# Performance work log

Measured on AMD Instinct MI355X. Metric: run time of the kernel, lower is better.

Reference implementation:

```python
import jax, jax.numpy as jnp
import numpy as np

T = 1_000_000  # sequence length
H = 5          # LSTM hidden size
NC = 4         # number of channel streams (all fed through lstm1, as in the original)


def setup_inputs() -> dict:
    key = jax.random.key(0)
    ks = jax.random.split(key, 14)
    s = 1.0 / np.sqrt(H)  # PyTorch default LSTM/Linear init scale
    u = lambda k, shape: jax.random.uniform(k, shape, jnp.float32, -s, s)
    sf1 = 1.0 / np.sqrt(20.0)
    sf2 = 1.0 / np.sqrt(10.0)
    return {
        "inputs": jax.random.normal(ks[0], (T, 1, NC), jnp.float32),
        # lstm1 layer 0: input_size=1
        "w_ih0": u(ks[1], (4 * H, 1)),
        "w_hh0": u(ks[2], (4 * H, H)),
        "b_ih0": u(ks[3], (4 * H,)),
        "b_hh0": u(ks[4], (4 * H,)),
        # lstm1 layer 1: input_size=H
        "w_ih1": u(ks[5], (4 * H, H)),
        "w_hh1": u(ks[6], (4 * H, H)),
        "b_ih1": u(ks[7], (4 * H,)),
        "b_hh1": u(ks[8], (4 * H,)),
        "fc1_w": jax.random.uniform(ks[9], (10, 20), jnp.float32, -sf1, sf1),
        "fc1_b": jax.random.uniform(ks[10], (10,), jnp.float32, -sf1, sf1),
        "fc2_w": jax.random.uniform(ks[11], (1, 10), jnp.float32, -sf2, sf2),
        "fc2_b": jax.random.uniform(ks[12], (1,), jnp.float32, -sf2, sf2),
    }


def _lstm_layer(x_seq, w_ih, w_hh, b_ih, b_hh):
    """Single PyTorch-style LSTM layer. x_seq: (T, B, in) -> h_seq: (T, B, H)."""
    # Input projection for all timesteps at once (outside the scan).
    gx = jnp.einsum('tbi,gi->tbg', x_seq, w_ih) + b_ih + b_hh  # (T, B, 4H)

    def step(carry, gx_t):
        h, c = carry
        g = gx_t + h @ w_hh.T                      # (B, 4H)
        i, f, gg, o = jnp.split(g, 4, axis=-1)     # PyTorch gate order i,f,g,o
        i = jax.nn.sigmoid(i)
        f = jax.nn.sigmoid(f)
        gg = jnp.tanh(gg)
        o = jax.nn.sigmoid(o)
        c = f * c + i * gg
        h = o * jnp.tanh(c)
        return (h, c), h

    B = x_seq.shape[1]
    z = jnp.zeros((B, H), x_seq.dtype)
    _, h_seq = jax.lax.scan(step, (z, z), gx)
    return h_seq


def reference(inputs, w_ih0, w_hh0, b_ih0, b_hh0, w_ih1, w_hh1, b_ih1, b_hh1,
              fc1_w, fc1_b, fc2_w, fc2_b):
    # Original code runs all 4 channel streams through lstm1 (lstm2-4 unused),
    # so we fold the 4 streams into the LSTM batch dim: (T, 4, 1).
    x = inputs[:, 0, :, None]                      # (T, NC, 1)
    h = _lstm_layer(x, w_ih0, w_hh0, b_ih0, b_hh0)  # (T, NC, H)
    h = _lstm_layer(h, w_ih1, w_hh1, b_ih1, b_hh1)  # (T, NC, H)
    # torch.cat((out1..out4), dim=2) on (T,1,H) slices == channel-major reshape
    out_cat = h.reshape(T, 1, NC * H)              # (T, 1, 20)
    out = out_cat @ fc1_w.T + fc1_b                # (T, 1, 10)
    out = out @ fc2_w.T + fc2_b                    # (T, 1, 1)
    return out
```

## Files before the change

kernel.cpp:

```cpp
#include <hip/hip_runtime.h>

#define T_TOTAL 1000000
#define NCHUNK  9216
#define CLEN    109
#define WARM    24


typedef float v2 __attribute__((ext_vector_type(2)));

#define L2E  1.44269504088896340736f
#define K2   2.88539008177792681472f

__device__ __forceinline__ float bperm(int addr4, float v) {
    return __int_as_float(__builtin_amdgcn_ds_bpermute(addr4, __float_as_int(v)));
}
__device__ __forceinline__ v2 pkfma(v2 a, v2 b, v2 c) {
    return __builtin_elementwise_fma(a, b, c);
}

__global__ __launch_bounds__(64, 1) void lstm_chunks(
    const float* __restrict__ inp,
    const float* __restrict__ wih0,
    const float* __restrict__ whh0,
    const float* __restrict__ bih0,
    const float* __restrict__ bhh0,
    const float* __restrict__ wih1,
    const float* __restrict__ whh1,
    const float* __restrict__ bih1,
    const float* __restrict__ bhh1,
    const float* __restrict__ fc1w,
    const float* __restrict__ fc1b,
    const float* __restrict__ fc2w,
    const float* __restrict__ fc2b,
    float* __restrict__ out)
{
    const int lane = threadIdx.x & 63;
    int cw = lane / 20; if (cw > 2) cw = 2;
    int q  = lane - cw * 20; if (q > 19) q = 19;
    const int b = q / 5;
    const int j = q % 5;
    const int chunk = blockIdx.x * 3 + cw;
    const int base  = cw * 20;

    int gh[5];
    #pragma unroll
    for (int k = 0; k < 5; ++k) gh[k] = (base + b * 5 + k) * 4;
    const int rd5  = (lane + 5)  * 4;
    const int rd10 = (lane + 10) * 4;

    v2 W0x01, W0x23, BB001, BB023, BB101, BB123;
    v2 W0h01[5], W0h23[5], W1a01[5], W1a23[5], W1b01[5], W1b23[5];
    {
        const int r0 = j, r1 = 5 + j, r2 = 10 + j, r3 = 15 + j;
        const v2 s01 = v2{-L2E, -L2E};
        const v2 s23 = v2{-K2,  -L2E};
        W0x01 = s01 * v2{wih0[r0], wih0[r1]};
        W0x23 = s23 * v2{wih0[r2], wih0[r3]};
        BB001 = s01 * v2{bih0[r0] + bhh0[r0], bih0[r1] + bhh0[r1]};
        BB023 = s23 * v2{bih0[r2] + bhh0[r2], bih0[r3] + bhh0[r3]};
        BB101 = s01 * v2{bih1[r0] + bhh1[r0], bih1[r1] + bhh1[r1]};
        BB123 = s23 * v2{bih1[r2] + bhh1[r2], bih1[r3] + bhh1[r3]};
        #pragma unroll
        for (int k = 0; k < 5; ++k) {
            W0h01[k] = s01 * v2{whh0[r0 * 5 + k], whh0[r1 * 5 + k]};
            W0h23[k] = s23 * v2{whh0[r2 * 5 + k], whh0[r3 * 5 + k]};
            W1a01[k] = s01 * v2{wih1[r0 * 5 + k], wih1[r1 * 5 + k]};
            W1a23[k] = s23 * v2{wih1[r2 * 5 + k], wih1[r3 * 5 + k]};
            W1b01[k] = s01 * v2{whh1[r0 * 5 + k], whh1[r1 * 5 + k]};
            W1b23[k] = s23 * v2{whh1[r2 * 5 + k], whh1[r3 * 5 + k]};
        }
    }
    float vb[5] = {0, 0, 0, 0, 0};
    float sc = fc2b[0];
    #pragma unroll
    for (int m = 0; m < 10; ++m) {
        const float f2 = fc2w[m];
        sc = __builtin_fmaf(f2, fc1b[m], sc);
        #pragma unroll
        for (int k = 0; k < 5; ++k)
            vb[k] = __builtin_fmaf(f2, fc1w[m * 20 + b * 5 + k], vb[k]);
    }

    const int o_begin = chunk * CLEN;
    const int warm = (chunk == 0) ? 0 : WARM;

    float C0 = 0.0f, C1 = 0.0f;
    float h0r[5] = {0, 0, 0, 0, 0};
    float h1r[5] = {0, 0, 0, 0, 0};

    auto ldx = [&](int t) -> float {
        const int tt = (t > T_TOTAL - 1) ? (T_TOTAL - 1) : t;
        return inp[(size_t)tt * 4 + b];
    };

    auto cellp = [&](v2 A01, v2 A23, float& C) -> float {
        const float ei = __builtin_amdgcn_exp2f(A01.x);
        const float ef = __builtin_amdgcn_exp2f(A01.y);
        const float eg = __builtin_amdgcn_exp2f(A23.x);
        const float eo = __builtin_amdgcn_exp2f(A23.y);
        const float Di = 1.0f + ei, Df = 1.0f + ef, Dg = 1.0f + eg, Do = 1.0f + eo;
        const float p1 = Di * Df, p2 = Dg * Do, p3 = Df * Do;
        const float r  = __builtin_amdgcn_rcpf(p1 * p2);
        const float f  = (Di * p2) * r;
        const float o  = (p1 * Dg) * r;
        const float tg = __builtin_fmaf(K2, eg, -K2);
        C = __builtin_fmaf(f, C, (tg * p3) * r);
        const float eh = __builtin_amdgcn_exp2f(C);
        return (o * (1.0f - eh)) * __builtin_amdgcn_rcpf(1.0f + eh);
    };

    auto matvec0 = [&](float x, const float (&h)[5], v2& A01, v2& A23) {
        const v2 xx = v2{x, x};
        v2 P01 = pkfma(W0x01, xx, BB001);
        v2 P23 = pkfma(W0x23, xx, BB023);
        const v2 k0 = v2{h[0], h[0]}, k1 = v2{h[1], h[1]};
        const v2 k2 = v2{h[2], h[2]}, k3 = v2{h[3], h[3]};
        const v2 k4 = v2{h[4], h[4]};
        P01 = pkfma(W0h01[0], k0, P01);  v2 Q01 = W0h01[2] * k2;
        P23 = pkfma(W0h23[0], k0, P23);  v2 Q23 = W0h23[2] * k2;
        P01 = pkfma(W0h01[1], k1, P01);  Q01 = pkfma(W0h01[3], k3, Q01);
        P23 = pkfma(W0h23[1], k1, P23);  Q23 = pkfma(W0h23[3], k3, Q23);
        Q01 = pkfma(W0h01[4], k4, Q01);
        Q23 = pkfma(W0h23[4], k4, Q23);
        A01 = P01 + Q01; A23 = P23 + Q23;
    };
    auto matvec1 = [&](const float (&h0)[5], const float (&h1)[5], v2& A01, v2& A23) {
        v2 P01 = BB101, P23 = BB123;
        const v2 g0 = v2{h1[0], h1[0]};
        v2 Q01 = W1b01[0] * g0;
        v2 Q23 = W1b23[0] * g0;
        #pragma unroll
        for (int k = 0; k < 5; ++k) {
            const v2 hk = v2{h0[k], h0[k]};
            P01 = pkfma(W1a01[k], hk, P01);
            P23 = pkfma(W1a23[k], hk, P23);
        }
        #pragma unroll
        for (int k = 1; k < 5; ++k) {
            const v2 gk = v2{h1[k], h1[k]};
            Q01 = pkfma(W1b01[k], gk, Q01);
            Q23 = pkfma(W1b23[k], gk, Q23);
        }
        A01 = P01 + Q01; A23 = P23 + Q23;
    };

    int t = o_begin - warm;
    {
        v2 A01, A23;
        matvec0(ldx(t), h0r, A01, A23);
        const float h0 = cellp(A01, A23, C0);
        #pragma unroll
        for (int k = 0; k < 5; ++k) h0r[k] = bperm(gh[k], h0);
    }
    float xc = ldx(t + 1);

    #define BODY(EMIT)                                                         \
    {                                                                          \
        v2 A01, A23;                                                           \
        matvec1(h0r, h1r, A01, A23);                                           \
        const float h1 = cellp(A01, A23, C1);                                  \
        float h1n[5];                                                          \
        _Pragma("unroll")                                                      \
        for (int k = 0; k < 5; ++k) h1n[k] = bperm(gh[k], h1);                 \
        const float xn = ldx(t + 2);                                           \
        matvec0(xc, h0r, A01, A23);                                            \
        const float h0 = cellp(A01, A23, C0);                                  \
        _Pragma("unroll")                                                      \
        for (int k = 0; k < 5; ++k) h0r[k] = bperm(gh[k], h0);                 \
        xc = xn;                                                               \
        if (EMIT) {                                                            \
            float p = vb[0] * h1n[0];                                          \
            p = __builtin_fmaf(vb[1], h1n[1], p);                              \
            p = __builtin_fmaf(vb[2], h1n[2], p);                              \
            p = __builtin_fmaf(vb[3], h1n[3], p);                              \
            p = __builtin_fmaf(vb[4], h1n[4], p);                              \
            const float u = p + bperm(rd5, p);                                 \
            const float S = u + bperm(rd10, u);                                \
            if (q == 0 && t < T_TOTAL) out[t] = S + sc;                        \
        }                                                                      \
        _Pragma("unroll")                                                      \
        for (int k = 0; k < 5; ++k) h1r[k] = h1n[k];                           \
    }

    for (int i = 0; i < warm; ++i, ++t) BODY(false)
    for (int i = 0; i < CLEN; ++i, ++t) BODY(true)

    #undef BODY
}

extern "C" void kernel_launch(void* const* d_in, const int* in_sizes, int n_in,
                              void* d_out, int out_size, void* d_ws, size_t ws_size,
                              hipStream_t stream) {
    (void)in_sizes; (void)n_in; (void)d_ws; (void)ws_size; (void)out_size;
    lstm_chunks<<<NCHUNK / 3, 64, 0, stream>>>(
        (const float*)d_in[0],  (const float*)d_in[1],  (const float*)d_in[2],
        (const float*)d_in[3],  (const float*)d_in[4],  (const float*)d_in[5],
        (const float*)d_in[6],  (const float*)d_in[7],  (const float*)d_in[8],
        (const float*)d_in[9],  (const float*)d_in[10], (const float*)d_in[11],
        (const float*)d_in[12], (float*)d_out);
}
```

Measured before the change: 181.0 us.

## Replace packed FMA matvecs with scalar FMAs and use fewer, longer chunks

The packed two-wide FMA vector math in the gate matvecs is replaced by plain scalar FMA chains, one accumulator per gate. The chunk decomposition also changes from 9216 chunks of 109 steps with 24 warmup steps to 6144 chunks of 164 steps with 16 warmup steps. Fewer chunks and shorter warmup cut redundant recurrent work but lengthen the serial chain each wave runs. The reduced warmup may also lower accuracy at chunk boundaries, and the scalar code issues roughly twice as many FMA instructions.

```diff
diff --git a/kernel.cpp b/kernel.cpp
--- a/kernel.cpp
+++ b/kernel.cpp
@@ -1,12 +1,10 @@
 #include <hip/hip_runtime.h>
 
 #define T_TOTAL 1000000
-#define NCHUNK  9216
-#define CLEN    109
-#define WARM    24
-
-
-typedef float v2 __attribute__((ext_vector_type(2)));
+#define NCHUNK  6144
+#define CLEN    164
+#define WARM    16
+
 
 #define L2E  1.44269504088896340736f
 #define K2   2.88539008177792681472f
@@ -14,8 +12,8 @@
 __device__ __forceinline__ float bperm(int addr4, float v) {
     return __int_as_float(__builtin_amdgcn_ds_bpermute(addr4, __float_as_int(v)));
 }
-__device__ __forceinline__ v2 pkfma(v2 a, v2 b, v2 c) {
-    return __builtin_elementwise_fma(a, b, c);
+__device__ __forceinline__ float fmaf_(float a, float b, float c) {
+    return __builtin_fmaf(a, b, c);
 }
 
 __global__ __launch_bounds__(64, 1) void lstm_chunks(
@@ -48,26 +46,23 @@
     const int rd5  = (lane + 5)  * 4;
     const int rd10 = (lane + 10) * 4;
 
-    v2 W0x01, W0x23, BB001, BB023, BB101, BB123;
-    v2 W0h01[5], W0h23[5], W1a01[5], W1a23[5], W1b01[5], W1b23[5];
+    float Wx[4], BB0[4], BB1[4];
+    float W0[4][5], Wa[4][5], Wb[4][5];
     {
-        const int r0 = j, r1 = 5 + j, r2 = 10 + j, r3 = 15 + j;
-        const v2 s01 = v2{-L2E, -L2E};
-        const v2 s23 = v2{-K2,  -L2E};
-        W0x01 = s01 * v2{wih0[r0], wih0[r1]};
-        W0x23 = s23 * v2{wih0[r2], wih0[r3]};
-        BB001 = s01 * v2{bih0[r0] + bhh0[r0], bih0[r1] + bhh0[r1]};
-        BB023 = s23 * v2{bih0[r2] + bhh0[r2], bih0[r3] + bhh0[r3]};
-        BB101 = s01 * v2{bih1[r0] + bhh1[r0], bih1[r1] + bhh1[r1]};
-        BB123 = s23 * v2{bih1[r2] + bhh1[r2], bih1[r3] + bhh1[r3]};
-        #pragma unroll
-        for (int k = 0; k < 5; ++k) {
-            W0h01[k] = s01 * v2{whh0[r0 * 5 + k], whh0[r1 * 5 + k]};
-            W0h23[k] = s23 * v2{whh0[r2 * 5 + k], whh0[r3 * 5 + k]};
-            W1a01[k] = s01 * v2{wih1[r0 * 5 + k], wih1[r1 * 5 + k]};
-            W1a23[k] = s23 * v2{wih1[r2 * 5 + k], wih1[r3 * 5 + k]};
-            W1b01[k] = s01 * v2{whh1[r0 * 5 + k], whh1[r1 * 5 + k]};
-            W1b23[k] = s23 * v2{whh1[r2 * 5 + k], whh1[r3 * 5 + k]};
+        const float sg[4] = {-L2E, -L2E, -K2, -L2E};
+        #pragma unroll
+        for (int g = 0; g < 4; ++g) {
+            const int row = g * 5 + j;
+            const float s = sg[g];
+            Wx[g]  = s * wih0[row];
+            BB0[g] = s * (bih0[row] + bhh0[row]);
+            BB1[g] = s * (bih1[row] + bhh1[row]);
+            #pragma unroll
+            for (int k = 0; k < 5; ++k) {
+                W0[g][k] = s * whh0[row * 5 + k];
+                Wa[g][k] = s * wih1[row * 5 + k];
+                Wb[g][k] = s * whh1[row * 5 + k];
+            }
         }
     }
     float vb[5] = {0, 0, 0, 0, 0};
@@ -75,10 +70,10 @@
     #pragma unroll
     for (int m = 0; m < 10; ++m) {
         const float f2 = fc2w[m];
-        sc = __builtin_fmaf(f2, fc1b[m], sc);
+        sc = fmaf_(f2, fc1b[m], sc);
         #pragma unroll
         for (int k = 0; k < 5; ++k)
-            vb[k] = __builtin_fmaf(f2, fc1w[m * 20 + b * 5 + k], vb[k]);
+            vb[k] = fmaf_(f2, fc1w[m * 20 + b * 5 + k], vb[k]);
     }
 
     const int o_begin = chunk * CLEN;
@@ -93,62 +88,66 @@
         return inp[(size_t)tt * 4 + b];
     };
 
-    auto cellp = [&](v2 A01, v2 A23, float& C) -> float {
-        const float ei = __builtin_amdgcn_exp2f(A01.x);
-        const float ef = __builtin_amdgcn_exp2f(A01.y);
-        const float eg = __builtin_amdgcn_exp2f(A23.x);
-        const float eo = __builtin_amdgcn_exp2f(A23.y);
+    auto cellp = [&](float a0, float a1, float a2, float a3, float& C) -> float {
+        const float ei = __builtin_amdgcn_exp2f(a0);
+        const float ef = __builtin_amdgcn_exp2f(a1);
+        const float eg = __builtin_amdgcn_exp2f(a2);
+        const float eo = __builtin_amdgcn_exp2f(a3);
         const float Di = 1.0f + ei, Df = 1.0f + ef, Dg = 1.0f + eg, Do = 1.0f + eo;
         const float p1 = Di * Df, p2 = Dg * Do, p3 = Df * Do;
         const float r  = __builtin_amdgcn_rcpf(p1 * p2);
         const float f  = (Di * p2) * r;
         const float o  = (p1 * Dg) * r;
-        const float tg = __builtin_fmaf(K2, eg, -K2);
-        C = __builtin_fmaf(f, C, (tg * p3) * r);
+        const float tg = fmaf_(K2, eg, -K2);
+        C = fmaf_(f, C, (tg * p3) * r);
         const float eh = __builtin_amdgcn_exp2f(C);
         return (o * (1.0f - eh)) * __builtin_amdgcn_rcpf(1.0f + eh);
     };
 
-    auto matvec0 = [&](float x, const float (&h)[5], v2& A01, v2& A23) {
-        const v2 xx = v2{x, x};
-        v2 P01 = pkfma(W0x01, xx, BB001);
-        v2 P23 = pkfma(W0x23, xx, BB023);
-        const v2 k0 = v2{h[0], h[0]}, k1 = v2{h[1], h[1]};
-        const v2 k2 = v2{h[2], h[2]}, k3 = v2{h[3], h[3]};
-        const v2 k4 = v2{h[4], h[4]};
-        P01 = pkfma(W0h01[0], k0, P01);  v2 Q01 = W0h01[2] * k2;
-        P23 = pkfma(W0h23[0], k0, P23);  v2 Q23 = W0h23[2] * k2;
-        P01 = pkfma(W0h01[1], k1, P01);  Q01 = pkfma(W0h01[3], k3, Q01);
-        P23 = pkfma(W0h23[1], k1, P23);  Q23 = pkfma(W0h23[3], k3, Q23);
-        Q01 = pkfma(W0h01[4], k4, Q01);
-        Q23 = pkfma(W0h23[4], k4, Q23);
-        A01 = P01 + Q01; A23 = P23 + Q23;
-    };
-    auto matvec1 = [&](const float (&h0)[5], const float (&h1)[5], v2& A01, v2& A23) {
-        v2 P01 = BB101, P23 = BB123;
-        const v2 g0 = v2{h1[0], h1[0]};
-        v2 Q01 = W1b01[0] * g0;
-        v2 Q23 = W1b23[0] * g0;
+    auto matvec0 = [&](float x, const float (&h)[5],
+                       float& a0, float& a1, float& a2, float& a3) {
+        float t0 = fmaf_(Wx[0], x, BB0[0]);
+        float t1 = fmaf_(Wx[1], x, BB0[1]);
+        float t2 = fmaf_(Wx[2], x, BB0[2]);
+        float t3 = fmaf_(Wx[3], x, BB0[3]);
         #pragma unroll
         for (int k = 0; k < 5; ++k) {
-            const v2 hk = v2{h0[k], h0[k]};
-            P01 = pkfma(W1a01[k], hk, P01);
-            P23 = pkfma(W1a23[k], hk, P23);
+            t0 = fmaf_(W0[0][k], h[k], t0);
+            t1 = fmaf_(W0[1][k], h[k], t1);
+            t2 = fmaf_(W0[2][k], h[k], t2);
+            t3 = fmaf_(W0[3][k], h[k], t3);
+        }
+        a0 = t0; a1 = t1; a2 = t2; a3 = t3;
+    };
+    auto matvec1 = [&](const float (&h0)[5], const float (&h1)[5],
+                       float& a0, float& a1, float& a2, float& a3) {
+        float t0 = BB1[0], t1 = BB1[1], t2 = BB1[2], t3 = BB1[3];
+        float u0 = Wb[0][0] * h1[0];
+        float u1 = Wb[1][0] * h1[0];
+        float u2 = Wb[2][0] * h1[0];
+        float u3 = Wb[3][0] * h1[0];
+        #pragma unroll
+        for (int k = 0; k < 5; ++k) {
+            t0 = fmaf_(Wa[0][k], h0[k], t0);
+            t1 = fmaf_(Wa[1][k], h0[k], t1);
+            t2 = fmaf_(Wa[2][k], h0[k], t2);
+            t3 = fmaf_(Wa[3][k], h0[k], t3);
         }
         #pragma unroll
         for (int k = 1; k < 5; ++k) {
-            const v2 gk = v2{h1[k], h1[k]};
-            Q01 = pkfma(W1b01[k], gk, Q01);
-            Q23 = pkfma(W1b23[k], gk, Q23);
-        }
-        A01 = P01 + Q01; A23 = P23 + Q23;
+            u0 = fmaf_(Wb[0][k], h1[k], u0);
+            u1 = fmaf_(Wb[1][k], h1[k], u1);
+            u2 = fmaf_(Wb[2][k], h1[k], u2);
+            u3 = fmaf_(Wb[3][k], h1[k], u3);
+        }
+        a0 = t0 + u0; a1 = t1 + u1; a2 = t2 + u2; a3 = t3 + u3;
     };
 
     int t = o_begin - warm;
     {
-        v2 A01, A23;
-        matvec0(ldx(t), h0r, A01, A23);
-        const float h0 = cellp(A01, A23, C0);
+        float a0, a1, a2, a3;
+        matvec0(ldx(t), h0r, a0, a1, a2, a3);
+        const float h0 = cellp(a0, a1, a2, a3, C0);
         #pragma unroll
         for (int k = 0; k < 5; ++k) h0r[k] = bperm(gh[k], h0);
     }
@@ -156,24 +155,24 @@
 
     #define BODY(EMIT)                                                         \
     {                                                                          \
-        v2 A01, A23;                                                           \
-        matvec1(h0r, h1r, A01, A23);                                           \
-        const float h1 = cellp(A01, A23, C1);                                  \
+        float a0, a1, a2, a3;                                                  \
+        matvec1(h0r, h1r, a0, a1, a2, a3);                                     \
+        const float h1 = cellp(a0, a1, a2, a3, C1);                            \
         float h1n[5];                                                          \
         _Pragma("unroll")                                                      \
         for (int k = 0; k < 5; ++k) h1n[k] = bperm(gh[k], h1);                 \
         const float xn = ldx(t + 2);                                           \
-        matvec0(xc, h0r, A01, A23);                                            \
-        const float h0 = cellp(A01, A23, C0);                                  \
+        matvec0(xc, h0r, a0, a1, a2, a3);                                      \
+        const float h0 = cellp(a0, a1, a2, a3, C0);                            \
         _Pragma("unroll")                                                      \
         for (int k = 0; k < 5; ++k) h0r[k] = bperm(gh[k], h0);                 \
         xc = xn;                                                               \
         if (EMIT) {                                                            \
             float p = vb[0] * h1n[0];                                          \
-            p = __builtin_fmaf(vb[1], h1n[1], p);                              \
-            p = __builtin_fmaf(vb[2], h1n[2], p);                              \
-            p = __builtin_fmaf(vb[3], h1n[3], p);                              \
-            p = __builtin_fmaf(vb[4], h1n[4], p);                              \
+            p = fmaf_(vb[1], h1n[1], p);                                       \
+            p = fmaf_(vb[2], h1n[2], p);                                       \
+            p = fmaf_(vb[3], h1n[3], p);                                       \
+            p = fmaf_(vb[4], h1n[4], p);                                       \
             const float u = p + bperm(rd5, p);                                 \
             const float S = u + bperm(rd10, u);                                \
             if (q == 0 && t < T_TOTAL) out[t] = S + sc;                        \
```

Result: slower. 192.8 us (+6.5%).
